# Performance work log

Hardware: AMD Instinct MI355X
Metric: run time of the kernel (lower is better)

Reference implementation:

```python
import jax, jax.numpy as jnp
import numpy as np

DIM = 1024
N_HEADS = 16
HEAD_DIM = DIM // N_HEADS
MLP_DIM = 4096
B, L, M = 4, 1024, 1024
EPS = 1e-5


def _mha(q_in, k_in, v_in, mask, wq, wk, wv, wo):
    b, l, d = q_in.shape
    m = k_in.shape[1]
    # torch view(b, l, head_dim, n_heads): split last dim as (head_dim, n_heads)
    q = (q_in @ wq).reshape(b, l, HEAD_DIM, N_HEADS)
    k = (k_in @ wk).reshape(b, m, HEAD_DIM, N_HEADS)
    v = (v_in @ wv).reshape(b, m, HEAD_DIM, N_HEADS)  # computed but unused downstream (source quirk)
    score = jnp.einsum('bldn,bmdn->blmn', q, k)
    # source applies mask BEFORE scaling
    score = jnp.where(mask, jnp.float32(-1e9), score)
    score = score / (HEAD_DIM ** 0.5)
    attn = jax.nn.softmax(score, axis=2)
    # SOURCE QUIRK: second einsum uses k, not v — reproduced faithfully
    x = jnp.einsum('blmn,bmdn->bldn', attn, k)
    x = x.reshape(b, l, d)  # 'b l d n -> b l (d n)'
    return x @ wo


def _layer_norm(x, g, b):
    mu = jnp.mean(x, axis=-1, keepdims=True)
    var = jnp.var(x, axis=-1, keepdims=True)
    return (x - mu) * jax.lax.rsqrt(var + EPS) * g + b


def setup_inputs() -> dict:
    key = jax.random.key(0)
    ks = jax.random.split(key, 16)
    s = 0.02
    inp = {
        'x': jax.random.normal(ks[0], (B, L, DIM), dtype=jnp.float32),
        'enc_output': jax.random.normal(ks[1], (B, M, DIM), dtype=jnp.float32),
        # causal mask: True above diagonal => masked
        'self_attn_mask': jnp.triu(jnp.ones((L, L), dtype=bool), k=1)[None, :, :, None],
        'enc_dec_mask': jnp.zeros((1, L, M, 1), dtype=bool),
        'sa_wq': s * jax.random.normal(ks[2], (DIM, DIM), jnp.float32),
        'sa_wk': s * jax.random.normal(ks[3], (DIM, DIM), jnp.float32),
        'sa_wv': s * jax.random.normal(ks[4], (DIM, DIM), jnp.float32),
        'sa_wo': s * jax.random.normal(ks[5], (DIM, DIM), jnp.float32),
        'ca_wq': s * jax.random.normal(ks[6], (DIM, DIM), jnp.float32),
        'ca_wk': s * jax.random.normal(ks[7], (DIM, DIM), jnp.float32),
        'ca_wv': s * jax.random.normal(ks[8], (DIM, DIM), jnp.float32),
        'ca_wo': s * jax.random.normal(ks[9], (DIM, DIM), jnp.float32),
        'ln1_g': jnp.ones((DIM,), jnp.float32), 'ln1_b': jnp.zeros((DIM,), jnp.float32),
        'ln2_g': jnp.ones((DIM,), jnp.float32), 'ln2_b': jnp.zeros((DIM,), jnp.float32),
        'ln3_g': jnp.ones((DIM,), jnp.float32), 'ln3_b': jnp.zeros((DIM,), jnp.float32),
        'ff_w1': s * jax.random.normal(ks[10], (DIM, MLP_DIM), jnp.float32),
        'ff_b1': jnp.zeros((MLP_DIM,), jnp.float32),
        'ff_w2': s * jax.random.normal(ks[11], (MLP_DIM, DIM), jnp.float32),
        'ff_b2': jnp.zeros((DIM,), jnp.float32),
    }
    return inp


def reference(x, enc_output, self_attn_mask, enc_dec_mask,
              sa_wq, sa_wk, sa_wv, sa_wo,
              ca_wq, ca_wk, ca_wv, ca_wo,
              ln1_g, ln1_b, ln2_g, ln2_b, ln3_g, ln3_b,
              ff_w1, ff_b1, ff_w2, ff_b2):
    # self-attention + residual + LN (dropout = identity in eval)
    h = x + _mha(x, x, x, self_attn_mask, sa_wq, sa_wk, sa_wv, sa_wo)
    h = _layer_norm(h, ln1_g, ln1_b)
    # encoder-decoder attention + residual + LN
    h = h + _mha(h, enc_output, enc_output, enc_dec_mask, ca_wq, ca_wk, ca_wv, ca_wo)
    h = _layer_norm(h, ln2_g, ln2_b)
    # position-wise FFN (gelu, exact erf like torch default) + residual + LN
    ff = jax.nn.gelu(h @ ff_w1 + ff_b1, approximate=False) @ ff_w2 + ff_b2
    h = h + ff
    h = _layer_norm(h, ln3_g, ln3_b)
    return h
```

## Files before the change

### kernel.cpp

```cpp
#include <hip/hip_runtime.h>
#include <hip/hip_bf16.h>
#include <stdint.h>

typedef unsigned short u16;
typedef _Float16 f16x8 __attribute__((ext_vector_type(8)));
typedef float f32x4 __attribute__((ext_vector_type(4)));

#define TOK 4096

__device__ __forceinline__ u16 f2h(float f) {
  _Float16 h = (_Float16)f;
  return __builtin_bit_cast(unsigned short, h);
}
__device__ __forceinline__ float h2f(u16 b) {
  return (float)__builtin_bit_cast(_Float16, b);
}
__device__ __forceinline__ unsigned pack2(float a, float b) {
  return (unsigned)f2h(a) | ((unsigned)f2h(b) << 16);
}
__device__ __forceinline__ void gld16(const u16* g, u16* l) {
  __builtin_amdgcn_global_load_lds(
      (const __attribute__((address_space(1))) void*)g,
      (__attribute__((address_space(3))) void*)l, 16, 0, 0);
}
__device__ __forceinline__ float gelu_fast(float v) {
  float z = 1.5957691216f * v * (1.0f + 0.044715f * v * v);
  return v / (1.0f + __expf(-z));
}

__device__ __forceinline__ void tc_body(const float* W, u16* Wt, int K, int N,
                                        int bx, int by, int tid) {
  __shared__ float tile[32][33];
  int n0 = bx * 32, k0 = by * 32;
  int tx = tid & 31, ty = tid >> 5;
#pragma unroll
  for (int e = 0; e < 4; e++)
    tile[ty + e * 8][tx] = W[(size_t)(k0 + ty + e * 8) * N + n0 + tx];
  __syncthreads();
#pragma unroll
  for (int e = 0; e < 4; e++)
    Wt[(size_t)(n0 + ty + e * 8) * K + k0 + tx] = f2h(tile[tx][ty + e * 8]);
}
__device__ __forceinline__ void cast_body(const float* in, u16* out, int blk, int tid) {
  int i = blk * 256 + tid;
  const float4* p = (const float4*)(in + (size_t)i * 8);
  float4 a = p[0], b = p[1];
  uint4 o;
  o.x = pack2(a.x, a.y); o.y = pack2(a.z, a.w);
  o.z = pack2(b.x, b.y); o.w = pack2(b.z, b.w);
  *(uint4*)(out + (size_t)i * 8) = o;
}

__global__ __launch_bounds__(256) void prep_kernel(
    const float* x, const float* enc, u16* xh, u16* ench,
    const float* W0, const float* W1, const float* W2,
    const float* W3, const float* W4, const float* W5,
    u16* T0, u16* T1, u16* T2, u16* T3, u16* T4, u16* T5,
    const float* Wff1, u16* Tff1, const float* Wff2, u16* Tff2) {
  int blk = blockIdx.x, tid = threadIdx.x;
  if (blk < 2048) { cast_body(x, xh, blk, tid); return; }
  if (blk < 4096) { cast_body(enc, ench, blk - 2048, tid); return; }
  if (blk < 10240) {
    int t = blk - 4096;
    int z = t >> 10, s = t & 1023;
    const float* W; u16* T;
    switch (z) {
      case 0: W = W0; T = T0; break;
      case 1: W = W1; T = T1; break;
      case 2: W = W2; T = T2; break;
      case 3: W = W3; T = T3; break;
      case 4: W = W4; T = T4; break;
      default: W = W5; T = T5; break;
    }
    tc_body(W, T, 1024, 1024, s & 31, s >> 5, tid);
    return;
  }
  if (blk < 14336) {
    int t = blk - 10240;
    tc_body(Wff1, Tff1, 1024, 4096, t & 127, t >> 7, tid);
    return;
  }
  {
    int t = blk - 14336;
    tc_body(Wff2, Tff2, 4096, 1024, t & 31, t >> 5, tid);
  }
}

template <int EPI, int BN>
__global__ __launch_bounds__((BN == 256) ? 512 : 256)
void gemm_bt_kernel(const u16* __restrict__ A0,
                    const u16* __restrict__ A1,
                    const u16* __restrict__ Bt0,
                    const u16* __restrict__ Bt1,
                    u16* __restrict__ Cb0,
                    u16* __restrict__ Cb1,
                    u16* __restrict__ CbT,
                    const float* __restrict__ bias,
                    int M, int N, int K, int KLEN) {
  const u16* A  = (EPI == 0 && blockIdx.z) ? A1 : A0;
  const u16* Bt = (EPI == 0 && blockIdx.z) ? Bt1 : Bt0;
  u16* Cb = (EPI == 0 && blockIdx.z) ? Cb1 : Cb0;
  __shared__ u16 As[2][128 * 32];
  __shared__ u16 Bs[2][BN * 32];
  int tid = threadIdx.x, lane = tid & 63, wid = tid >> 6;
  int gx = gridDim.x, gy = gridDim.y;
  int nwg = gx * gy;
  int flat = blockIdx.x + gx * blockIdx.y;
  int k8 = flat & 7, idx = flat >> 3;
  int bx, by;
  if (gx >= 16) {
    int rx = gx >> 2, ry = gy >> 1;
    int kx = k8 & 3, ky = k8 >> 2;
    bx = kx * rx + idx % rx;
    by = ky * ry + idx / rx;
  } else {
    int widx = k8 * (nwg >> 3) + idx;
    bx = widx % gx;
    by = widx / gx;
  }
  int row0 = by * 128, col0 = bx * BN;
  int wm = (BN == 256) ? (wid >> 2) * 64 : (wid >> 1) * 64;
  int wn = (BN == 256) ? (wid & 3) * 64 : (wid & 1) * 64;
  int sr = tid >> 2;
  int scol = (((tid & 3) ^ (sr & 3)) * 8);
  size_t koff = (EPI == 4) ? (size_t)blockIdx.z * KLEN : 0;
  const u16* Ab0 = A + (size_t)(row0 + sr) * K + koff + scol;
  const u16* Ab1 = A + (size_t)(row0 + 64 + sr) * K + koff + scol;
  const u16* Bb0 = Bt + (size_t)(col0 + sr) * K + koff + scol;
  const u16* Bb1 = Bt + (size_t)(col0 + ((BN == 256) ? 128 : 64) + sr) * K + koff + scol;
  f32x4 acc[4][4];
#pragma unroll
  for (int i = 0; i < 4; i++)
#pragma unroll
    for (int j = 0; j < 4; j++) { acc[i][j][0] = 0.f; acc[i][j][1] = 0.f; acc[i][j][2] = 0.f; acc[i][j][3] = 0.f; }
  int KT = KLEN >> 5;
  int ra = lane & 15, kg = lane >> 4;
  int aoff[4], boff[4];
#pragma unroll
  for (int i = 0; i < 4; i++) {
    int r = wm + i * 16 + ra;
    aoff[i] = r * 32 + ((kg ^ (r & 3)) * 8);
    int c = wn + i * 16 + ra;
    boff[i] = c * 32 + ((kg ^ (c & 3)) * 8);
  }

  auto STAGE = [&](int kt, int buf) {
    if constexpr (BN == 256) {
      gld16(Ab0 + kt * 32, &As[buf][wid * 512]);
      gld16(Bb0 + kt * 32, &Bs[buf][wid * 512]);
      gld16(Bb1 + kt * 32, &Bs[buf][4096 + wid * 512]);
    } else {
      gld16(Ab0 + kt * 32, &As[buf][wid * 512]);
      gld16(Ab1 + kt * 32, &As[buf][2048 + wid * 512]);
      gld16(Bb0 + kt * 32, &Bs[buf][wid * 512]);
      gld16(Bb1 + kt * 32, &Bs[buf][2048 + wid * 512]);
    }
  };

  STAGE(0, 0);
  __syncthreads();
  int cur = 0;
  for (int kt = 0; kt < KT; ++kt) {
    if (kt + 1 < KT) STAGE(kt + 1, cur ^ 1);
    f16x8 af[4], bfv[4];
#pragma unroll
    for (int i = 0; i < 4; i++) af[i] = *(const f16x8*)&As[cur][aoff[i]];
#pragma unroll
    for (int j = 0; j < 4; j++) bfv[j] = *(const f16x8*)&Bs[cur][boff[j]];
#pragma unroll
    for (int i = 0; i < 4; i++)
#pragma unroll
      for (int j = 0; j < 4; j++)
        acc[i][j] = __builtin_amdgcn_mfma_f32_16x16x32_f16(af[i], bfv[j], acc[i][j], 0, 0, 0);
    __syncthreads();
    cur ^= 1;
  }

  int rq = kg * 4;
#pragma unroll
  for (int i = 0; i < 4; i++) {
    int rowb = row0 + wm + i * 16 + rq;
    if (EPI == 0) {
      int b = rowb >> 10, l0 = rowb & 1023;
      int d0 = (col0 + wn) >> 4;
      size_t hb = ((size_t)(b * 16 + ra)) * 1024;
      u16 h[4][4];
#pragma unroll
      for (int j = 0; j < 4; j++)
#pragma unroll
        for (int q = 0; q < 4; q++) h[j][q] = f2h(acc[i][j][q]);
#pragma unroll
      for (int q = 0; q < 4; q++) {
        ushort4 hv;
        hv.x = h[0][q]; hv.y = h[1][q]; hv.z = h[2][q]; hv.w = h[3][q];
        *(ushort4*)&Cb[(hb + l0 + q) * 64 + d0] = hv;
      }
      if (blockIdx.z) {
#pragma unroll
        for (int j = 0; j < 4; j++) {
          uint2 ov;
          ov.x = (unsigned)h[j][0] | ((unsigned)h[j][1] << 16);
          ov.y = (unsigned)h[j][2] | ((unsigned)h[j][3] << 16);
          *(uint2*)&CbT[(hb >> 10 << 16) + ((size_t)(d0 + j)) * 1024 + l0] = ov;
        }
      }
    } else {
#pragma unroll
      for (int j = 0; j < 4; j++) {
        int col = col0 + wn + j * 16 + ra;
        float bval = 0.f;
        if (EPI == 2) bval = bias[col];
        if (EPI == 4 && blockIdx.z == 0 && bias) bval = bias[col];
#pragma unroll
        for (int q = 0; q < 4; q++) {
          int row = rowb + q;
          float v = acc[i][j][q] + bval;
          if (EPI == 2) {
            Cb[(size_t)row * N + col] = f2h(gelu_fast(v));
          } else {
            Cb[(size_t)blockIdx.z * M * N + (size_t)row * N + col] = f2h(v);
          }
        }
      }
    }
  }
}

template <bool CAUSAL>
__global__ __launch_bounds__(256) void flash3_kernel(const u16* __restrict__ Qh,
                                                     const u16* __restrict__ Kh,
                                                     const u16* __restrict__ KhT,
                                                     u16* __restrict__ Xtok) {
  const int L = 1024;
  int tid = threadIdx.x, lane = tid & 63, wid = tid >> 6;
  int gx = gridDim.x, nwg = gx * gridDim.y;
  int flat = blockIdx.x + gx * blockIdx.y;
  int widx = (flat & 7) * (nwg >> 3) + (flat >> 3);
  int qt = widx % gx, bh = widx / gx;
  if (CAUSAL) qt = gx - 1 - qt;
  __shared__ u16 Ks[2][4096];
  __shared__ u16 Kt[2][4096];
  __shared__ u16 Ps[4][2048];
  int ra = lane & 15, kg = lane >> 4;
  int rq = kg * 4;
  int wr0 = qt * 128 + wid * 32;
  f16x8 qa[2][2];
#pragma unroll
  for (int i = 0; i < 2; i++) {
    const u16* Qb = Qh + ((size_t)bh * L + wr0 + i * 16 + ra) * 64;
    qa[i][0] = *(const f16x8*)(Qb + kg * 8);
    qa[i][1] = *(const f16x8*)(Qb + 32 + kg * 8);
  }
  f32x4 oacc[2][4];
#pragma unroll
  for (int i = 0; i < 2; i++)
#pragma unroll
    for (int d = 0; d < 4; d++) { oacc[i][d][0] = 0.f; oacc[i][d][1] = 0.f; oacc[i][d][2] = 0.f; oacc[i][d][3] = 0.f; }
  float l_i[2][4];
#pragma unroll
  for (int i = 0; i < 2; i++)
#pragma unroll
    for (int q = 0; q < 4; q++) l_i[i][q] = 0.f;
  int ntiles = CAUSAL ? (2 * qt + 2) : 16;
  int fr = lane >> 3, fc = lane & 7;

#define KSTAGE(mt, buf) do {                                                        \
    {                                                                               \
      int rr = wid * 8 + fr;                                                        \
      int cc = fc ^ fr;                                                             \
      gld16(Kh + ((size_t)bh * L + (mt) * 64 + rr) * 64 + cc * 8, &Ks[buf][wid * 512]);          \
      gld16(KhT + ((size_t)bh * 64 + rr) * L + (size_t)(mt) * 64 + cc * 8, &Kt[buf][wid * 512]); \
    }                                                                               \
    {                                                                               \
      int rr = 32 + wid * 8 + fr;                                                   \
      int cc = fc ^ fr;                                                             \
      gld16(Kh + ((size_t)bh * L + (mt) * 64 + rr) * 64 + cc * 8, &Ks[buf][2048 + wid * 512]);          \
      gld16(KhT + ((size_t)bh * 64 + rr) * L + (size_t)(mt) * 64 + cc * 8, &Kt[buf][2048 + wid * 512]); \
    }                                                                               \
  } while (0)

  KSTAGE(0, 0);
  __syncthreads();
  int cur = 0;
  for (int mt = 0; mt < ntiles; ++mt) {
    if (mt + 1 < ntiles) KSTAGE(mt + 1, cur ^ 1);
    bool active = !(CAUSAL && (wr0 + 31 < mt * 64));
    if (active) {
      bool wmask = CAUSAL && (mt * 64 + 63 > wr0);
      float p[2][4][4];
      __builtin_amdgcn_s_setprio(1);
#pragma unroll
      for (int j = 0; j < 4; j++) {
        int krow = j * 16 + ra;
        int s2 = krow & 7;
        f16x8 kb0 = *(const f16x8*)&Ks[cur][krow * 64 + ((kg ^ s2) * 8)];
        f16x8 kb1 = *(const f16x8*)&Ks[cur][krow * 64 + (((4 + kg) ^ s2) * 8)];
#pragma unroll
        for (int i = 0; i < 2; i++) {
          f32x4 a; a[0] = 0.f; a[1] = 0.f; a[2] = 0.f; a[3] = 0.f;
          a = __builtin_amdgcn_mfma_f32_16x16x32_f16(qa[i][0], kb0, a, 0, 0, 0);
          a = __builtin_amdgcn_mfma_f32_16x16x32_f16(qa[i][1], kb1, a, 0, 0, 0);
#pragma unroll
          for (int q = 0; q < 4; q++) {
            float v = a[q] * 0.125f;
            if (wmask) {
              int rg = wr0 + i * 16 + rq + q;
              int cg = mt * 64 + j * 16 + ra;
              if (cg > rg) v = -1.25e8f;
            }
            p[i][j][q] = __expf(v);
          }
        }
      }
      __builtin_amdgcn_s_setprio(0);
#pragma unroll
      for (int i = 0; i < 2; i++) {
        float rs[4] = {0.f, 0.f, 0.f, 0.f};
#pragma unroll
        for (int j = 0; j < 4; j++)
#pragma unroll
          for (int q = 0; q < 4; q++) rs[q] += p[i][j][q];
#pragma unroll
        for (int off = 1; off < 16; off <<= 1)
#pragma unroll
          for (int q = 0; q < 4; q++) rs[q] += __shfl_xor(rs[q], off);
#pragma unroll
        for (int q = 0; q < 4; q++) l_i[i][q] += rs[q];
      }
#pragma unroll
      for (int i = 0; i < 2; i++)
#pragma unroll
        for (int j = 0; j < 4; j++)
#pragma unroll
          for (int q = 0; q < 4; q++) {
            int prow = i * 16 + rq + q;
            int pcol = j * 16 + ra;
            Ps[wid][prow * 64 + (((pcol >> 3) ^ (prow & 7)) * 8) + (pcol & 7)] = f2h(p[i][j][q]);
          }
      f16x8 pa[2][2];
#pragma unroll
      for (int i = 0; i < 2; i++) {
        int arow = i * 16 + ra;
        int s3 = arow & 7;
        pa[i][0] = *(const f16x8*)&Ps[wid][arow * 64 + ((kg ^ s3) * 8)];
        pa[i][1] = *(const f16x8*)&Ps[wid][arow * 64 + (((4 + kg) ^ s3) * 8)];
      }
      __builtin_amdgcn_s_setprio(1);
#pragma unroll
      for (int d = 0; d < 4; d++) {
        int krow = d * 16 + ra;
        int s4 = krow & 7;
        f16x8 kc0 = *(const f16x8*)&Kt[cur][krow * 64 + ((kg ^ s4) * 8)];
        f16x8 kc1 = *(const f16x8*)&Kt[cur][krow * 64 + (((4 + kg) ^ s4) * 8)];
#pragma unroll
        for (int i = 0; i < 2; i++) {
          oacc[i][d] = __builtin_amdgcn_mfma_f32_16x16x32_f16(pa[i][0], kc0, oacc[i][d], 0, 0, 0);
          oacc[i][d] = __builtin_amdgcn_mfma_f32_16x16x32_f16(pa[i][1], kc1, oacc[i][d], 0, 0, 0);
        }
      }
      __builtin_amdgcn_s_setprio(0);
    }
    __syncthreads();
    cur ^= 1;
  }
#undef KSTAGE
  int b = bh >> 4, nh = bh & 15;
#pragma unroll
  for (int i = 0; i < 2; i++)
#pragma unroll
    for (int q = 0; q < 4; q++) {
      float inv = 1.0f / l_i[i][q];
      int l = wr0 + i * 16 + rq + q;
      size_t rowg = ((size_t)b * 1024 + l) * 1024;
#pragma unroll
      for (int d = 0; d < 4; d++)
        Xtok[rowg + (d * 16 + ra) * 16 + nh] = f2h(oacc[i][d][q] * inv);
    }
}

template <int WRITE_H, int P>
__global__ __launch_bounds__(256) void ln_kernel(const u16* __restrict__ parts,
                                                 const float* __restrict__ res,
                                                 const float* __restrict__ g,
                                                 const float* __restrict__ bb,
                                                 float* __restrict__ outf,
                                                 u16* __restrict__ outh) {
  int row = blockIdx.x, tid = threadIdx.x;
  int lane = tid & 63, wid = tid >> 6;
  size_t base = (size_t)row * 1024 + tid * 4;
  float4 vr = *(const float4*)(res + base);
  float x0 = vr.x, x1 = vr.y, x2 = vr.z, x3 = vr.w;
#pragma unroll
  for (int p = 0; p < P; p++) {
    uint2 v = *(const uint2*)&parts[(size_t)p * 4194304 + base];
    x0 += h2f((u16)v.x);
    x1 += h2f((u16)(v.x >> 16));
    x2 += h2f((u16)v.y);
    x3 += h2f((u16)(v.y >> 16));
  }
  float s = x0 + x1 + x2 + x3;
  float sq = x0 * x0 + x1 * x1 + x2 * x2 + x3 * x3;
#pragma unroll
  for (int off = 1; off < 64; off <<= 1) {
    s += __shfl_xor(s, off);
    sq += __shfl_xor(sq, off);
  }
  __shared__ float red[8];
  if (lane == 0) { red[wid] = s; red[4 + wid] = sq; }
  __syncthreads();
  s = red[0] + red[1] + red[2] + red[3];
  sq = red[4] + red[5] + red[6] + red[7];
  float mean = s * (1.0f / 1024.0f);
  float var = sq * (1.0f / 1024.0f) - mean * mean;
  float rstd = rsqrtf(var + 1e-5f);
  float4 vg = *(const float4*)(g + tid * 4);
  float4 vb = *(const float4*)(bb + tid * 4);
  float y0 = (x0 - mean) * rstd * vg.x + vb.x;
  float y1 = (x1 - mean) * rstd * vg.y + vb.y;
  float y2 = (x2 - mean) * rstd * vg.z + vb.z;
  float y3 = (x3 - mean) * rstd * vg.w + vb.w;
  float4 yo; yo.x = y0; yo.y = y1; yo.z = y2; yo.w = y3;
  *(float4*)(outf + base) = yo;
  if (WRITE_H) {
    uint2 ov; ov.x = pack2(y0, y1); ov.y = pack2(y2, y3);
    *(uint2*)(outh + base) = ov;
  }
}

extern "C" void kernel_launch(void* const* d_in, const int* in_sizes, int n_in,
                              void* d_out, int out_size, void* d_ws, size_t ws_size,
                              hipStream_t stream) {
  (void)in_sizes; (void)n_in; (void)out_size; (void)ws_size;
  const float* x    = (const float*)d_in[0];
  const float* enc  = (const float*)d_in[1];
  const float* sa_wq = (const float*)d_in[4];
  const float* sa_wk = (const float*)d_in[5];
  const float* sa_wo = (const float*)d_in[7];
  const float* ca_wq = (const float*)d_in[8];
  const float* ca_wk = (const float*)d_in[9];
  const float* ca_wo = (const float*)d_in[11];
  const float* ln1g = (const float*)d_in[12];
  const float* ln1b = (const float*)d_in[13];
  const float* ln2g = (const float*)d_in[14];
  const float* ln2b = (const float*)d_in[15];
  const float* ln3g = (const float*)d_in[16];
  const float* ln3b = (const float*)d_in[17];
  const float* ffw1 = (const float*)d_in[18];
  const float* ffb1 = (const float*)d_in[19];
  const float* ffw2 = (const float*)d_in[20];
  const float* ffb2 = (const float*)d_in[21];

  uint8_t* w = (uint8_t*)d_ws;
  const size_t MB = 1024ull * 1024ull;
  u16* wt_saq = (u16*)(w + 0 * MB);
  u16* wt_sak = (u16*)(w + 2 * MB);
  u16* wt_sao = (u16*)(w + 4 * MB);
  u16* wt_caq = (u16*)(w + 6 * MB);
  u16* wt_cak = (u16*)(w + 8 * MB);
  u16* wt_cao = (u16*)(w + 10 * MB);
  u16* wt_ff1 = (u16*)(w + 12 * MB);
  u16* wt_ff2 = (u16*)(w + 20 * MB);
  u16* act_h  = (u16*)(w + 28 * MB);
  u16* enc_h  = (u16*)(w + 36 * MB);
  u16* qhd    = (u16*)(w + 44 * MB);
  u16* khd    = (u16*)(w + 52 * MB);
  u16* khdT   = (u16*)(w + 60 * MB);
  u16* ctxtok = (u16*)(w + 68 * MB);
  u16* parts  = (u16*)(w + 76 * MB);
  float* hA   = (float*)(w + 108 * MB);
  float* hB   = (float*)(w + 124 * MB);
  u16* ff1h = qhd;

  prep_kernel<<<18432, 256, 0, stream>>>(
      x, enc, act_h, enc_h,
      sa_wq, sa_wk, sa_wo, ca_wq, ca_wk, ca_wo,
      wt_saq, wt_sak, wt_sao, wt_caq, wt_cak, wt_cao,
      ffw1, wt_ff1, ffw2, wt_ff2);

  gemm_bt_kernel<0, 128><<<dim3(8, 32, 2), 256, 0, stream>>>(
      act_h, act_h, wt_saq, wt_sak, qhd, khd, khdT, nullptr, TOK, 1024, 1024, 1024);
  flash3_kernel<true><<<dim3(8, 64), 256, 0, stream>>>(qhd, khd, khdT, ctxtok);
  gemm_bt_kernel<4, 128><<<dim3(8, 32, 2), 256, 0, stream>>>(
      ctxtok, ctxtok, wt_sao, wt_sao, parts, nullptr, nullptr, nullptr, TOK, 1024, 1024, 512);
  ln_kernel<1, 2><<<4096, 256, 0, stream>>>(parts, x, ln1g, ln1b, hA, act_h);

  gemm_bt_kernel<0, 128><<<dim3(8, 32, 2), 256, 0, stream>>>(
      act_h, enc_h, wt_caq, wt_cak, qhd, khd, khdT, nullptr, TOK, 1024, 1024, 1024);
  flash3_kernel<false><<<dim3(8, 64), 256, 0, stream>>>(qhd, khd, khdT, ctxtok);
  gemm_bt_kernel<4, 128><<<dim3(8, 32, 2), 256, 0, stream>>>(
      ctxtok, ctxtok, wt_cao, wt_cao, parts, nullptr, nullptr, nullptr, TOK, 1024, 1024, 512);
  ln_kernel<1, 2><<<4096, 256, 0, stream>>>(parts, hA, ln2g, ln2b, hB, act_h);

  gemm_bt_kernel<2, 256><<<dim3(16, 32, 1), 512, 0, stream>>>(
      act_h, act_h, wt_ff1, wt_ff1, ff1h, nullptr, nullptr, ffb1, TOK, 4096, 1024, 1024);
  gemm_bt_kernel<4, 128><<<dim3(8, 32, 4), 256, 0, stream>>>(
      ff1h, ff1h, wt_ff2, wt_ff2, parts, nullptr, nullptr, ffb2, TOK, 1024, 4096, 1024);
  ln_kernel<0, 4><<<4096, 256, 0, stream>>>(parts, hB, ln3g, ln3b, (float*)d_out, nullptr);
}
```

Baseline: 362.9 us.

## Concatenate Q/K weights into one GEMM, change LDS swizzle, halve FF2 split-K

Q and K projection weights are stored contiguously so the projection runs as one N=2048 GEMM over a 16x32 grid instead of a z=2 launch, with the output buffer chosen per column tile. The LDS XOR swizzle now uses (row>>1)&3 instead of row&3, aiming to reduce bank conflicts on the 16-byte fragment reads. FF2 split-K drops from 4 to 2 partitions, which cuts partial-sum traffic and LN reduction work but gives fewer workgroups and longer K loops per block.

Result: faster. 353.9 us (-2.5%).

```diff
diff --git a/kernel.cpp b/kernel.cpp
--- a/kernel.cpp
+++ b/kernel.cpp
@@ -90,16 +90,12 @@
 __global__ __launch_bounds__((BN == 256) ? 512 : 256)
 void gemm_bt_kernel(const u16* __restrict__ A0,
                     const u16* __restrict__ A1,
-                    const u16* __restrict__ Bt0,
-                    const u16* __restrict__ Bt1,
+                    const u16* __restrict__ Bt,
                     u16* __restrict__ Cb0,
                     u16* __restrict__ Cb1,
                     u16* __restrict__ CbT,
                     const float* __restrict__ bias,
                     int M, int N, int K, int KLEN) {
-  const u16* A  = (EPI == 0 && blockIdx.z) ? A1 : A0;
-  const u16* Bt = (EPI == 0 && blockIdx.z) ? Bt1 : Bt0;
-  u16* Cb = (EPI == 0 && blockIdx.z) ? Cb1 : Cb0;
   __shared__ u16 As[2][128 * 32];
   __shared__ u16 Bs[2][BN * 32];
   int tid = threadIdx.x, lane = tid & 63, wid = tid >> 6;
@@ -119,10 +115,12 @@
     by = widx / gx;
   }
   int row0 = by * 128, col0 = bx * BN;
+  bool is_k = (EPI == 0) && (col0 >= 1024);
+  const u16* A = is_k ? A1 : A0;
   int wm = (BN == 256) ? (wid >> 2) * 64 : (wid >> 1) * 64;
   int wn = (BN == 256) ? (wid & 3) * 64 : (wid & 1) * 64;
   int sr = tid >> 2;
-  int scol = (((tid & 3) ^ (sr & 3)) * 8);
+  int scol = (((tid & 3) ^ ((sr >> 1) & 3)) * 8);
   size_t koff = (EPI == 4) ? (size_t)blockIdx.z * KLEN : 0;
   const u16* Ab0 = A + (size_t)(row0 + sr) * K + koff + scol;
   const u16* Ab1 = A + (size_t)(row0 + 64 + sr) * K + koff + scol;
@@ -139,9 +137,9 @@
 #pragma unroll
   for (int i = 0; i < 4; i++) {
     int r = wm + i * 16 + ra;
-    aoff[i] = r * 32 + ((kg ^ (r & 3)) * 8);
+    aoff[i] = r * 32 + ((kg ^ ((r >> 1) & 3)) * 8);
     int c = wn + i * 16 + ra;
-    boff[i] = c * 32 + ((kg ^ (c & 3)) * 8);
+    boff[i] = c * 32 + ((kg ^ ((c >> 1) & 3)) * 8);
   }
 
   auto STAGE = [&](int kt, int buf) {
@@ -182,8 +180,9 @@
     int rowb = row0 + wm + i * 16 + rq;
     if (EPI == 0) {
       int b = rowb >> 10, l0 = rowb & 1023;
-      int d0 = (col0 + wn) >> 4;
+      int d0 = ((col0 + wn) >> 4) & 63;
       size_t hb = ((size_t)(b * 16 + ra)) * 1024;
+      u16* dst = is_k ? Cb1 : Cb0;
       u16 h[4][4];
 #pragma unroll
       for (int j = 0; j < 4; j++)
@@ -193,15 +192,15 @@
       for (int q = 0; q < 4; q++) {
         ushort4 hv;
         hv.x = h[0][q]; hv.y = h[1][q]; hv.z = h[2][q]; hv.w = h[3][q];
-        *(ushort4*)&Cb[(hb + l0 + q) * 64 + d0] = hv;
-      }
-      if (blockIdx.z) {
+        *(ushort4*)&dst[(hb + l0 + q) * 64 + d0] = hv;
+      }
+      if (is_k) {
 #pragma unroll
         for (int j = 0; j < 4; j++) {
           uint2 ov;
           ov.x = (unsigned)h[j][0] | ((unsigned)h[j][1] << 16);
           ov.y = (unsigned)h[j][2] | ((unsigned)h[j][3] << 16);
-          *(uint2*)&CbT[(hb >> 10 << 16) + ((size_t)(d0 + j)) * 1024 + l0] = ov;
+          *(uint2*)&CbT[((size_t)(b * 16 + ra)) * 65536 + ((size_t)(d0 + j)) * 1024 + l0] = ov;
         }
       }
     } else {
@@ -216,9 +215,9 @@
           int row = rowb + q;
           float v = acc[i][j][q] + bval;
           if (EPI == 2) {
-            Cb[(size_t)row * N + col] = f2h(gelu_fast(v));
+            Cb0[(size_t)row * N + col] = f2h(gelu_fast(v));
           } else {
-            Cb[(size_t)blockIdx.z * M * N + (size_t)row * N + col] = f2h(v);
+            Cb0[(size_t)blockIdx.z * M * N + (size_t)row * N + col] = f2h(v);
           }
         }
       }
@@ -452,48 +451,47 @@
 
   uint8_t* w = (uint8_t*)d_ws;
   const size_t MB = 1024ull * 1024ull;
-  u16* wt_saq = (u16*)(w + 0 * MB);
-  u16* wt_sak = (u16*)(w + 2 * MB);
-  u16* wt_sao = (u16*)(w + 4 * MB);
-  u16* wt_caq = (u16*)(w + 6 * MB);
-  u16* wt_cak = (u16*)(w + 8 * MB);
-  u16* wt_cao = (u16*)(w + 10 * MB);
-  u16* wt_ff1 = (u16*)(w + 12 * MB);
-  u16* wt_ff2 = (u16*)(w + 20 * MB);
-  u16* act_h  = (u16*)(w + 28 * MB);
-  u16* enc_h  = (u16*)(w + 36 * MB);
-  u16* qhd    = (u16*)(w + 44 * MB);
-  u16* khd    = (u16*)(w + 52 * MB);
-  u16* khdT   = (u16*)(w + 60 * MB);
-  u16* ctxtok = (u16*)(w + 68 * MB);
-  u16* parts  = (u16*)(w + 76 * MB);
-  float* hA   = (float*)(w + 108 * MB);
-  float* hB   = (float*)(w + 124 * MB);
+  u16* wt_saqk = (u16*)(w + 0 * MB);
+  u16* wt_sao  = (u16*)(w + 4 * MB);
+  u16* wt_caqk = (u16*)(w + 6 * MB);
+  u16* wt_cao  = (u16*)(w + 10 * MB);
+  u16* wt_ff1  = (u16*)(w + 12 * MB);
+  u16* wt_ff2  = (u16*)(w + 20 * MB);
+  u16* act_h   = (u16*)(w + 28 * MB);
+  u16* enc_h   = (u16*)(w + 36 * MB);
+  u16* qhd     = (u16*)(w + 44 * MB);
+  u16* khd     = (u16*)(w + 52 * MB);
+  u16* khdT    = (u16*)(w + 60 * MB);
+  u16* ctxtok  = (u16*)(w + 68 * MB);
+  u16* parts   = (u16*)(w + 76 * MB);
+  float* hA    = (float*)(w + 108 * MB);
+  float* hB    = (float*)(w + 124 * MB);
   u16* ff1h = qhd;
 
   prep_kernel<<<18432, 256, 0, stream>>>(
       x, enc, act_h, enc_h,
       sa_wq, sa_wk, sa_wo, ca_wq, ca_wk, ca_wo,
-      wt_saq, wt_sak, wt_sao, wt_caq, wt_cak, wt_cao,
+      wt_saqk, wt_saqk + 1024 * 1024, wt_sao,
+      wt_caqk, wt_caqk + 1024 * 1024, wt_cao,
       ffw1, wt_ff1, ffw2, wt_ff2);
 
-  gemm_bt_kernel<0, 128><<<dim3(8, 32, 2), 256, 0, stream>>>(
-      act_h, act_h, wt_saq, wt_sak, qhd, khd, khdT, nullptr, TOK, 1024, 1024, 1024);
+  gemm_bt_kernel<0, 128><<<dim3(16, 32, 1), 256, 0, stream>>>(
+      act_h, act_h, wt_saqk, qhd, khd, khdT, nullptr, TOK, 2048, 1024, 1024);
   flash3_kernel<true><<<dim3(8, 64), 256, 0, stream>>>(qhd, khd, khdT, ctxtok);
   gemm_bt_kernel<4, 128><<<dim3(8, 32, 2), 256, 0, stream>>>(
-      ctxtok, ctxtok, wt_sao, wt_sao, parts, nullptr, nullptr, nullptr, TOK, 1024, 1024, 512);
+      ctxtok, ctxtok, wt_sao, parts, nullptr, nullptr, nullptr, TOK, 1024, 1024, 512);
   ln_kernel<1, 2><<<4096, 256, 0, stream>>>(parts, x, ln1g, ln1b, hA, act_h);
 
-  gemm_bt_kernel<0, 128><<<dim3(8, 32, 2), 256, 0, stream>>>(
-      act_h, enc_h, wt_caq, wt_cak, qhd, khd, khdT, nullptr, TOK, 1024, 1024, 1024);
+  gemm_bt_kernel<0, 128><<<dim3(16, 32, 1), 256, 0, stream>>>(
+      act_h, enc_h, wt_caqk, qhd, khd, khdT, nullptr, TOK, 2048, 1024, 1024);
   flash3_kernel<false><<<dim3(8, 64), 256, 0, stream>>>(qhd, khd, khdT, ctxtok);
   gemm_bt_kernel<4, 128><<<dim3(8, 32, 2), 256, 0, stream>>>(
-      ctxtok, ctxtok, wt_cao, wt_cao, parts, nullptr, nullptr, nullptr, TOK, 1024, 1024, 512);
+      ctxtok, ctxtok, wt_cao, parts, nullptr, nullptr, nullptr, TOK, 1024, 1024, 512);
   ln_kernel<1, 2><<<4096, 256, 0, stream>>>(parts, hA, ln2g, ln2b, hB, act_h);
 
   gemm_bt_kernel<2, 256><<<dim3(16, 32, 1), 512, 0, stream>>>(
-      act_h, act_h, wt_ff1, wt_ff1, ff1h, nullptr, nullptr, ffb1, TOK, 4096, 1024, 1024);
-  gemm_bt_kernel<4, 128><<<dim3(8, 32, 4), 256, 0, stream>>>(
-      ff1h, ff1h, wt_ff2, wt_ff2, parts, nullptr, nullptr, ffb2, TOK, 1024, 4096, 1024);
-  ln_kernel<0, 4><<<4096, 256, 0, stream>>>(parts, hB, ln3g, ln3b, (float*)d_out, nullptr);
-}
+      act_h, act_h, wt_ff1, ff1h, nullptr, nullptr, ffb1, TOK, 4096, 1024, 1024);
+  gemm_bt_kernel<4, 128><<<dim3(8, 32, 2), 256, 0, stream>>>(
+      ff1h, ff1h, wt_ff2, parts, nullptr, nullptr, ffb2, TOK, 1024, 4096, 2048);
+  ln_kernel<0, 2><<<4096, 256, 0, stream>>>(parts, hB, ln3g, ln3b, (float*)d_out, nullptr);
+}
```
